# Performance work log

Measured on AMD Instinct MI355X. Metric: run time of the kernel, lower is better.

The kernel has to match this reference:

```python
import jax, jax.numpy as jnp
import numpy as np

N_NODES = 50000
N_EDGES = 800000
FEAT, HID, OUT = 256, 256, 40
N_BATCH = 10000
BN_EPS = 1e-5
DEN_EPS = 1e-16


def setup_inputs() -> dict:
    key = jax.random.key(0)
    ks = jax.random.split(key, 12)
    # small feature scale keeps gaussian kernel exp(-gamma*||dh||^2) well-conditioned
    features = jax.random.normal(ks[0], (N_NODES, FEAT), dtype=jnp.float32) * 0.05
    edge_index = jax.random.randint(ks[1], (2, N_EDGES), 0, N_NODES, dtype=jnp.int64)
    batch_nodes = jax.random.randint(ks[2], (N_BATCH,), 0, N_NODES, dtype=jnp.int64)
    W1 = jax.random.normal(ks[3], (FEAT, HID), dtype=jnp.float32) / np.sqrt(FEAT)
    b1 = jnp.zeros((HID,), dtype=jnp.float32)
    gamma1 = jnp.float32(0.5)
    W2 = jax.random.normal(ks[4], (HID, OUT), dtype=jnp.float32) / np.sqrt(HID)
    b2 = jnp.zeros((OUT,), dtype=jnp.float32)
    gamma2 = jnp.float32(0.5)
    bn1_w = jnp.ones((HID,), dtype=jnp.float32)
    bn1_b = jnp.zeros((HID,), dtype=jnp.float32)
    bn2_w = jnp.ones((OUT,), dtype=jnp.float32)
    bn2_b = jnp.zeros((OUT,), dtype=jnp.float32)
    return dict(features=features, edge_index=edge_index, batch_nodes=batch_nodes,
                W1=W1, b1=b1, gamma1=gamma1, W2=W2, b2=b2, gamma2=gamma2,
                bn1_w=bn1_w, bn1_b=bn1_b, bn2_w=bn2_w, bn2_b=bn2_b)


def pfgcn_conv(x, edge_index, W, b, gamma):
    # linear transform then gaussian-kernel weighted aggregation over edges
    h = x @ W + b                                  # [N, C_out]
    src, dst = edge_index[0], edge_index[1]
    h_src = h[src]                                 # [E, C_out] gather
    h_dst = h[dst]                                 # [E, C_out] gather
    d2 = jnp.sum((h_src - h_dst) ** 2, axis=-1)    # [E]
    w = jnp.exp(-gamma * d2)                       # gaussian edge kernel
    denom = jax.ops.segment_sum(w, dst, num_segments=N_NODES) + DEN_EPS   # [N]
    num = jax.ops.segment_sum(w[:, None] * h_src, dst, num_segments=N_NODES)  # [N, C_out]
    return num / denom[:, None]


def batchnorm(x, g, b):
    # training-mode BatchNorm1d over the node dimension
    mu = jnp.mean(x, axis=0)
    var = jnp.var(x, axis=0)
    return (x - mu) * jax.lax.rsqrt(var + BN_EPS) * g + b


def reference(features, edge_index, batch_nodes, W1, b1, gamma1, W2, b2, gamma2,
              bn1_w, bn1_b, bn2_w, bn2_b):
    x = pfgcn_conv(features, edge_index, W1, b1, gamma1)
    x = jax.nn.relu(batchnorm(x, bn1_w, bn1_b))
    # dropout treated as identity (eval / deterministic reference)
    x = pfgcn_conv(x, edge_index, W2, b2, gamma2)
    x = jax.nn.relu(batchnorm(x, bn2_w, bn2_b))
    return jax.nn.log_softmax(x[batch_nodes], axis=1)
```

## Files before the change

### kernel.cpp

```cpp
#include <hip/hip_runtime.h>
#include <math.h>

#define N_NODES 50000
#define N_EDGES 800000
#define OUTC 40
#define N_BATCH 10000
#define H2S 48
#define BKT 64
#define SP 16

typedef float f32x4 __attribute__((ext_vector_type(4)));
typedef short s16x8 __attribute__((ext_vector_type(8)));
typedef short s16x4 __attribute__((ext_vector_type(4)));

union Frag { s16x8 v; s16x4 h[2]; };

__device__ inline unsigned short f2bf(float f) {
    unsigned int u = __float_as_uint(f);
    u += 0x7fff + ((u >> 16) & 1);
    return (unsigned short)(u >> 16);
}
__device__ inline float lo16(unsigned int u) { return __uint_as_float(u << 16); }
__device__ inline float hi16(unsigned int u) { return __uint_as_float(u & 0xffff0000u); }
__device__ inline unsigned int pk2(float a, float b) {
    return (unsigned int)f2bf(a) | ((unsigned int)f2bf(b) << 16);
}
__device__ inline void unpk8(uint4 u, float* f) {
    f[0] = lo16(u.x); f[1] = hi16(u.x);
    f[2] = lo16(u.y); f[3] = hi16(u.y);
    f[4] = lo16(u.z); f[5] = hi16(u.z);
    f[6] = lo16(u.w); f[7] = hi16(u.w);
}

__global__ __launch_bounds__(256) void init_kernel(const float* __restrict__ W1,
                                                   unsigned short* __restrict__ W1T,
                                                   int* __restrict__ cur,
                                                   float* __restrict__ stats) {
    int b = blockIdx.x, t = threadIdx.x;
    if (b < 256) {
        W1T[(size_t)t * 256 + b] = f2bf(W1[(size_t)b * 256 + t]);
    } else if (b < 256 + 196) {
        int i = (b - 256) * 256 + t;
        if (i < N_NODES) cur[i] = 0;
    } else {
        int base = (b - 452) * 1184;
        for (int i = base + t; i < base + 1184; i += 256)
            if (i < 9472) stats[i] = 0.f;
    }
}

__global__ __launch_bounds__(256) void scatter_kernel(const int* __restrict__ ei,
                                                      int* __restrict__ cur,
                                                      unsigned short* __restrict__ srcs) {
    int e = blockIdx.x * 256 + threadIdx.x;
    if (e >= N_EDGES) return;
    int d = ei[N_EDGES + e];
    int pos = atomicAdd(&cur[d], 1);
    if (pos < BKT) srcs[(size_t)d * BKT + pos] = (unsigned short)ei[e];
}

#define LDA 40
__global__ __launch_bounds__(256) void gemm1_mfma(const float* __restrict__ A,
                                                  const unsigned short* __restrict__ BT,
                                                  const float* __restrict__ bias,
                                                  unsigned short* __restrict__ C) {
    __shared__ unsigned short As[128 * LDA];
    __shared__ unsigned short Bs[128 * LDA];
    int t = threadIdx.x;
    int lane = t & 63, wave = t >> 6;
    int ln = lane & 15, quad = lane >> 4;
    int row0 = blockIdx.x * 128;
    int col0 = blockIdx.y * 128;
    int m0 = (wave & 1) * 64, n0 = (wave >> 1) * 64;
    f32x4 acc[4][4];
    #pragma unroll
    for (int i = 0; i < 4; i++)
        #pragma unroll
        for (int j = 0; j < 4; j++) acc[i][j] = (f32x4){0.f, 0.f, 0.f, 0.f};
    int r = t >> 1, half = t & 1;

    for (int k0 = 0; k0 < 256; k0 += 32) {
        {
            int gr = row0 + r;
            float4 v[4];
            if (gr < N_NODES) {
                const float4* src = (const float4*)(A + (size_t)gr * 256 + k0 + half * 16);
                v[0] = src[0]; v[1] = src[1]; v[2] = src[2]; v[3] = src[3];
            } else {
                float4 z = make_float4(0.f, 0.f, 0.f, 0.f);
                v[0] = z; v[1] = z; v[2] = z; v[3] = z;
            }
            ushort4* dst = (ushort4*)&As[r * LDA + half * 16];
            #pragma unroll
            for (int q = 0; q < 4; q++) {
                ushort4 u;
                u.x = f2bf(v[q].x); u.y = f2bf(v[q].y);
                u.z = f2bf(v[q].z); u.w = f2bf(v[q].w);
                dst[q] = u;
            }
        }
        {
            const ushort4* src = (const ushort4*)(BT + (size_t)(col0 + r) * 256 + k0 + half * 16);
            ushort4* dst = (ushort4*)&Bs[r * LDA + half * 16];
            dst[0] = src[0]; dst[1] = src[1]; dst[2] = src[2]; dst[3] = src[3];
        }
        __syncthreads();
        Frag af[4], bf[4];
        #pragma unroll
        for (int i = 0; i < 4; i++) {
            int ar = m0 + i * 16 + ln;
            af[i].h[0] = *(const s16x4*)&As[ar * LDA + quad * 8];
            af[i].h[1] = *(const s16x4*)&As[ar * LDA + quad * 8 + 4];
            int br = n0 + i * 16 + ln;
            bf[i].h[0] = *(const s16x4*)&Bs[br * LDA + quad * 8];
            bf[i].h[1] = *(const s16x4*)&Bs[br * LDA + quad * 8 + 4];
        }
        #pragma unroll
        for (int i = 0; i < 4; i++)
            #pragma unroll
            for (int j = 0; j < 4; j++)
                acc[i][j] = __builtin_amdgcn_mfma_f32_16x16x32_bf16(af[i].v, bf[j].v, acc[i][j], 0, 0, 0);
        __syncthreads();
    }
    #pragma unroll
    for (int j = 0; j < 4; j++) {
        int gc = col0 + n0 + j * 16 + ln;
        float bv = bias[gc];
        #pragma unroll
        for (int i = 0; i < 4; i++) {
            int gb = row0 + m0 + i * 16 + quad * 4;
            #pragma unroll
            for (int rg = 0; rg < 4; rg++) {
                int gr = gb + rg;
                if (gr < N_NODES) C[(size_t)gr * 256 + gc] = f2bf(acc[i][j][rg] + bv);
            }
        }
    }
}

__global__ __launch_bounds__(256) void agg1_kernel(const unsigned short* __restrict__ h,
                                                   const int* __restrict__ degp,
                                                   const unsigned short* __restrict__ srcs,
                                                   const float* __restrict__ gamma_p,
                                                   unsigned short* __restrict__ x1) {
    int lane = threadIdx.x & 63;
    int node = blockIdx.x * 4 + (threadIdx.x >> 6);
    if (node >= N_NODES) return;
    int eslot = lane >> 4, cgrp = lane & 15;
    float g = gamma_p[0];
    float hd[16];
    {
        const uint4* hrow = (const uint4*)(h + (size_t)node * 256 + cgrp * 16);
        uint4 u0 = hrow[0], u1 = hrow[1];
        unpk8(u0, hd); unpk8(u1, hd + 8);
    }
    float acc[16];
    #pragma unroll
    for (int c = 0; c < 16; c++) acc[c] = 0.f;
    float den = 0.f;
    int beg = node << 6;
    int end = beg + degp[node];
    int n_it = (end - beg + 3) >> 2;
    for (int it = 0; it < n_it; it++) {
        int i = beg + it * 4 + eslot;
        bool valid = i < end;
        int s = valid ? (int)srcs[i] : node;
        const uint4* arow = (const uint4*)(h + (size_t)s * 256 + cgrp * 16);
        uint4 u0 = arow[0], u1 = arow[1];
        float av[16];
        unpk8(u0, av); unpk8(u1, av + 8);
        float d2 = 0.f;
        #pragma unroll
        for (int c = 0; c < 16; c++) { float d = av[c] - hd[c]; d2 = fmaf(d, d, d2); }
        d2 += __shfl_xor(d2, 1, 64);
        d2 += __shfl_xor(d2, 2, 64);
        d2 += __shfl_xor(d2, 4, 64);
        d2 += __shfl_xor(d2, 8, 64);
        float w = valid ? __expf(-g * d2) : 0.f;
        den += w;
        #pragma unroll
        for (int c = 0; c < 16; c++) acc[c] = fmaf(w, av[c], acc[c]);
    }
    #pragma unroll
    for (int m = 16; m < 64; m <<= 1) {
        den += __shfl_xor(den, m, 64);
        #pragma unroll
        for (int c = 0; c < 16; c++) acc[c] += __shfl_xor(acc[c], m, 64);
    }
    if (eslot == 0) {
        float inv = 1.f / (den + 1e-16f);
        float vv[16];
        #pragma unroll
        for (int c = 0; c < 16; c++) vv[c] = acc[c] * inv;
        uint4 oA = make_uint4(pk2(vv[0], vv[1]), pk2(vv[2], vv[3]),
                              pk2(vv[4], vv[5]), pk2(vv[6], vv[7]));
        uint4 oB = make_uint4(pk2(vv[8], vv[9]), pk2(vv[10], vv[11]),
                              pk2(vv[12], vv[13]), pk2(vv[14], vv[15]));
        uint4* o4 = (uint4*)(x1 + (size_t)node * 256 + cgrp * 16);
        o4[0] = oA; o4[1] = oB;
    }
}

__global__ __launch_bounds__(256) void stats1_kernel(const unsigned short* __restrict__ x,
                                                     float* __restrict__ sum,
                                                     float* __restrict__ sumsq) {
    __shared__ float ls[4][256], lq[4][256];
    int t = threadIdx.x;
    int cg = (t & 63) * 4;
    int rs = t >> 6;
    float s0 = 0.f, s1 = 0.f, s2 = 0.f, s3 = 0.f;
    float q0 = 0.f, q1 = 0.f, q2 = 0.f, q3 = 0.f;
    for (int r = blockIdx.x * 4 + rs; r < N_NODES; r += gridDim.x * 4) {
        uint2 u = *(const uint2*)(x + (size_t)r * 256 + cg);
        float v0 = lo16(u.x), v1 = hi16(u.x), v2 = lo16(u.y), v3 = hi16(u.y);
        s0 += v0; q0 = fmaf(v0, v0, q0);
        s1 += v1; q1 = fmaf(v1, v1, q1);
        s2 += v2; q2 = fmaf(v2, v2, q2);
        s3 += v3; q3 = fmaf(v3, v3, q3);
    }
    ls[rs][cg] = s0; ls[rs][cg + 1] = s1; ls[rs][cg + 2] = s2; ls[rs][cg + 3] = s3;
    lq[rs][cg] = q0; lq[rs][cg + 1] = q1; lq[rs][cg + 2] = q2; lq[rs][cg + 3] = q3;
    __syncthreads();
    float S = ls[0][t] + ls[1][t] + ls[2][t] + ls[3][t];
    float Q = lq[0][t] + lq[1][t] + lq[2][t] + lq[3][t];
    atomicAdd(&sum[t * SP], S);
    atomicAdd(&sumsq[t * SP], Q);
}

__global__ __launch_bounds__(256) void gemm2_kernel(const unsigned short* __restrict__ X,
                                                    const float* __restrict__ W2,
                                                    const float* __restrict__ bias,
                                                    const float* __restrict__ sum1,
                                                    const float* __restrict__ sumsq1,
                                                    const float* __restrict__ bg,
                                                    const float* __restrict__ bb,
                                                    unsigned short* __restrict__ H) {
    __shared__ float W2s[40 * 260];
    __shared__ float aas[256], bbs[256];
    int t = threadIdx.x;
    for (int i = t; i < 256 * 40; i += 256) {
        int k = i / 40, c = i % 40;
        W2s[c * 260 + k] = W2[i];
    }
    {
        const float invN = 1.f / N_NODES;
        float mu = sum1[t * SP] * invN;
        float var = sumsq1[t * SP] * invN - mu * mu;
        float rs = rsqrtf(var + 1e-5f) * bg[t];
        aas[t] = rs;
        bbs[t] = bb[t] - mu * rs;
    }
    __syncthreads();
    int slot = t >> 2, cg = t & 3;
    int rbase = blockIdx.x * 256 + slot;
    const uint2* xp[4];
    #pragma unroll
    for (int rr = 0; rr < 4; rr++) xp[rr] = (const uint2*)(X + (size_t)(rbase + rr * 64) * 256);
    float acc[4][10];
    #pragma unroll
    for (int rr = 0; rr < 4; rr++)
        #pragma unroll
        for (int i = 0; i < 10; i++) acc[rr][i] = 0.f;

    for (int k4 = 0; k4 < 64; k4++) {
        int k = k4 * 4;
        float4 a4 = *(const float4*)&aas[k];
        float4 b4 = *(const float4*)&bbs[k];
        float4 w4[10];
        #pragma unroll
        for (int i = 0; i < 10; i++) w4[i] = *(const float4*)&W2s[(cg * 10 + i) * 260 + k];
        #pragma unroll
        for (int rr = 0; rr < 4; rr++) {
            uint2 xu = xp[rr][k4];
            float y0 = fmaxf(fmaf(lo16(xu.x), a4.x, b4.x), 0.f);
            float y1 = fmaxf(fmaf(hi16(xu.x), a4.y, b4.y), 0.f);
            float y2 = fmaxf(fmaf(lo16(xu.y), a4.z, b4.z), 0.f);
            float y3 = fmaxf(fmaf(hi16(xu.y), a4.w, b4.w), 0.f);
            #pragma unroll
            for (int i = 0; i < 10; i++)
                acc[rr][i] += y0 * w4[i].x + y1 * w4[i].y + y2 * w4[i].z + y3 * w4[i].w;
        }
    }
    #pragma unroll
    for (int rr = 0; rr < 4; rr++) {
        int row = rbase + rr * 64;
        if (row < N_NODES) {
            float y[10];
            #pragma unroll
            for (int i = 0; i < 10; i++) y[i] = acc[rr][i] + bias[cg * 10 + i];
            unsigned int* o32 = (unsigned int*)(H + (size_t)row * H2S + cg * 10);
            #pragma unroll
            for (int i = 0; i < 5; i++) o32[i] = pk2(y[2 * i], y[2 * i + 1]);
            if (cg == 1)
                *(uint4*)(H + (size_t)row * H2S + 40) = make_uint4(0, 0, 0, 0);
        }
    }
}

__global__ __launch_bounds__(256) void agg2_kernel(const unsigned short* __restrict__ h,
                                                   const int* __restrict__ degp,
                                                   const unsigned short* __restrict__ srcs,
                                                   const float* __restrict__ gamma_p,
                                                   float* __restrict__ x2) {
    int l32 = threadIdx.x & 31;
    int node = blockIdx.x * 8 + (threadIdx.x >> 5);
    if (node >= N_NODES) return;
    int eslot = l32 >> 3, cgrp = l32 & 7;
    float g = gamma_p[0];
    float hd[6];
    {
        const unsigned int* hrow = (const unsigned int*)(h + (size_t)node * H2S + cgrp * 6);
        unsigned int u0 = hrow[0], u1 = hrow[1], u2 = hrow[2];
        hd[0] = lo16(u0); hd[1] = hi16(u0);
        hd[2] = lo16(u1); hd[3] = hi16(u1);
        hd[4] = lo16(u2); hd[5] = hi16(u2);
    }
    float acc[6] = {0.f, 0.f, 0.f, 0.f, 0.f, 0.f};
    float den = 0.f;
    int beg = node << 6;
    int end = beg + degp[node];
    int n_it = (end - beg + 3) >> 2;
    for (int it = 0; it < n_it; it++) {
        int i = beg + it * 4 + eslot;
        bool valid = i < end;
        int s = valid ? (int)srcs[i] : node;
        const unsigned int* arow = (const unsigned int*)(h + (size_t)s * H2S + cgrp * 6);
        unsigned int u0 = arow[0], u1 = arow[1], u2 = arow[2];
        float av[6];
        av[0] = lo16(u0); av[1] = hi16(u0);
        av[2] = lo16(u1); av[3] = hi16(u1);
        av[4] = lo16(u2); av[5] = hi16(u2);
        float d2 = 0.f;
        #pragma unroll
        for (int j = 0; j < 6; j++) { float d = av[j] - hd[j]; d2 = fmaf(d, d, d2); }
        d2 += __shfl_xor(d2, 1, 64);
        d2 += __shfl_xor(d2, 2, 64);
        d2 += __shfl_xor(d2, 4, 64);
        float w = valid ? __expf(-g * d2) : 0.f;
        den += w;
        #pragma unroll
        for (int j = 0; j < 6; j++) acc[j] = fmaf(w, av[j], acc[j]);
    }
    #pragma unroll
    for (int m = 8; m < 32; m <<= 1) {
        den += __shfl_xor(den, m, 64);
        #pragma unroll
        for (int j = 0; j < 6; j++) acc[j] += __shfl_xor(acc[j], m, 64);
    }
    if (eslot == 0) {
        float inv = 1.f / (den + 1e-16f);
        int cb = cgrp * 6;
        #pragma unroll
        for (int j = 0; j < 6; j++)
            if (cb + j < OUTC) x2[(size_t)node * OUTC + cb + j] = acc[j] * inv;
    }
}

__global__ __launch_bounds__(256) void stats2_kernel(const float* __restrict__ x,
                                                     float* __restrict__ sum,
                                                     float* __restrict__ sumsq) {
    __shared__ float ls[12][40], lq[12][40];
    int t = threadIdx.x;
    if (t < 240) {
        int c2 = (t % 20) * 2;
        int rs = t / 20;
        float s0 = 0.f, s1 = 0.f, q0 = 0.f, q1 = 0.f;
        for (int r = blockIdx.x * 12 + rs; r < N_NODES; r += gridDim.x * 12) {
            float2 v = *(const float2*)(x + (size_t)r * OUTC + c2);
            s0 += v.x; q0 = fmaf(v.x, v.x, q0);
            s1 += v.y; q1 = fmaf(v.y, v.y, q1);
        }
        ls[rs][c2] = s0; ls[rs][c2 + 1] = s1;
        lq[rs][c2] = q0; lq[rs][c2 + 1] = q1;
    }
    __syncthreads();
    if (t < OUTC) {
        float S = 0.f, Q = 0.f;
        #pragma unroll
        for (int rs = 0; rs < 12; rs++) { S += ls[rs][t]; Q += lq[rs][t]; }
        atomicAdd(&sum[t * SP], S);
        atomicAdd(&sumsq[t * SP], Q);
    }
}

__global__ __launch_bounds__(256) void final_kernel(const float* __restrict__ x2,
                                                    const float* __restrict__ sum,
                                                    const float* __restrict__ sumsq,
                                                    const float* __restrict__ g,
                                                    const float* __restrict__ b,
                                                    const int* __restrict__ batch,
                                                    float* __restrict__ out) {
    int lane = threadIdx.x & 63;
    int row = blockIdx.x * 4 + (threadIdx.x >> 6);
    if (row >= N_BATCH) return;
    int node = batch[row];
    bool act = lane < OUTC;
    float v = -INFINITY;
    if (act) {
        const float invN = 1.f / N_NODES;
        float mu = sum[lane * SP] * invN;
        float var = sumsq[lane * SP] * invN - mu * mu;
        float xv = x2[(size_t)node * OUTC + lane];
        float y = (xv - mu) * rsqrtf(var + 1e-5f) * g[lane] + b[lane];
        v = fmaxf(y, 0.f);
    }
    float m = v;
    #pragma unroll
    for (int s = 1; s < 64; s <<= 1) m = fmaxf(m, __shfl_xor(m, s, 64));
    float p = act ? expf(v - m) : 0.f;
    float ssum = p;
    #pragma unroll
    for (int s = 1; s < 64; s <<= 1) ssum += __shfl_xor(ssum, s, 64);
    if (act) out[(size_t)row * OUTC + lane] = v - m - logf(ssum);
}

extern "C" void kernel_launch(void* const* d_in, const int* in_sizes, int n_in,
                              void* d_out, int out_size, void* d_ws, size_t ws_size,
                              hipStream_t stream) {
    const float* feat   = (const float*)d_in[0];
    const int*   ei     = (const int*)d_in[1];
    const int*   batch  = (const int*)d_in[2];
    const float* W1     = (const float*)d_in[3];
    const float* b1     = (const float*)d_in[4];
    const float* gamma1 = (const float*)d_in[5];
    const float* W2     = (const float*)d_in[6];
    const float* b2     = (const float*)d_in[7];
    const float* gamma2 = (const float*)d_in[8];
    const float* bn1w   = (const float*)d_in[9];
    const float* bn1b   = (const float*)d_in[10];
    const float* bn2w   = (const float*)d_in[11];
    const float* bn2b   = (const float*)d_in[12];

    char* ws = (char*)d_ws;
    unsigned short* h1  = (unsigned short*)ws;
    unsigned short* x1  = (unsigned short*)(ws + 25600000);
    unsigned short* srcs = (unsigned short*)(ws + 52000000);
    int* cur            = (int*)(ws + 65600000);
    float* stats        = (float*)(ws + 66000000);
    unsigned short* w1t = (unsigned short*)(ws + 76800000);
    float* sum1   = stats;
    float* sumsq1 = stats + 256 * SP;
    float* sum2   = stats + 512 * SP;
    float* sumsq2 = stats + 512 * SP + 40 * SP;
    unsigned short* h2 = (unsigned short*)ws;
    float* x2 = (float*)(ws + 25600000);
    float* out = (float*)d_out;

    init_kernel<<<460, 256, 0, stream>>>(W1, w1t, cur, stats);
    scatter_kernel<<<(N_EDGES + 255) / 256, 256, 0, stream>>>(ei, cur, srcs);

    gemm1_mfma<<<dim3(391, 2), 256, 0, stream>>>(feat, w1t, b1, h1);
    agg1_kernel<<<(N_NODES + 3) / 4, 256, 0, stream>>>(h1, cur, srcs, gamma1, x1);
    stats1_kernel<<<256, 256, 0, stream>>>(x1, sum1, sumsq1);

    gemm2_kernel<<<196, 256, 0, stream>>>(x1, W2, b2, sum1, sumsq1, bn1w, bn1b, h2);
    agg2_kernel<<<(N_NODES + 7) / 8, 256, 0, stream>>>(h2, cur, srcs, gamma2, x2);
    stats2_kernel<<<256, 256, 0, stream>>>(x2, sum2, sumsq2);
    final_kernel<<<(N_BATCH + 3) / 4, 256, 0, stream>>>(x2, sum2, sumsq2, bn2w, bn2b, batch, out);
}
```

Baseline: 347.6 us.

## Pre-convert features to bf16 in scatter kernel and spread gemm2 over more blocks

The fp32 to bf16 conversion of the node features moves out of gemm1 into extra blocks appended to the edge-scatter launch. The bf16 copy goes into the workspace buffer that x1 uses later. gemm1 then loads bf16 directly, halving its A-tile traffic, though the separate conversion pass adds a full read and write of the features. gemm2 drops from four rows per thread to one and launches 784 blocks instead of 196, for more parallelism at the cost of reloading W2 and the BN parameters into shared memory per block.

Result: slower. 360.3 us (+3.6%).

```diff
diff --git a/kernel.cpp b/kernel.cpp
--- a/kernel.cpp
+++ b/kernel.cpp
@@ -8,6 +8,8 @@
 #define H2S 48
 #define BKT 64
 #define SP 16
+#define SCAT_BLKS 3125
+#define CONV_BLKS 6250
 
 typedef float f32x4 __attribute__((ext_vector_type(4)));
 typedef short s16x8 __attribute__((ext_vector_type(8)));
@@ -49,18 +51,32 @@
     }
 }
 
-__global__ __launch_bounds__(256) void scatter_kernel(const int* __restrict__ ei,
-                                                      int* __restrict__ cur,
-                                                      unsigned short* __restrict__ srcs) {
-    int e = blockIdx.x * 256 + threadIdx.x;
-    if (e >= N_EDGES) return;
-    int d = ei[N_EDGES + e];
-    int pos = atomicAdd(&cur[d], 1);
-    if (pos < BKT) srcs[(size_t)d * BKT + pos] = (unsigned short)ei[e];
+__global__ __launch_bounds__(256) void scatter_conv(const int* __restrict__ ei,
+                                                    int* __restrict__ cur,
+                                                    unsigned short* __restrict__ srcs,
+                                                    const float* __restrict__ feat,
+                                                    unsigned short* __restrict__ fbf) {
+    int b = blockIdx.x, t = threadIdx.x;
+    if (b < SCAT_BLKS) {
+        int e = b * 256 + t;
+        if (e < N_EDGES) {
+            int d = ei[N_EDGES + e];
+            int pos = atomicAdd(&cur[d], 1);
+            if (pos < BKT) srcs[(size_t)d * BKT + pos] = (unsigned short)ei[e];
+        }
+    } else {
+        size_t e8 = ((size_t)(b - SCAT_BLKS) * 256 + t) * 8;
+        const float4* src = (const float4*)(feat + e8);
+        float4 v0 = src[0], v1 = src[1];
+        uint4 o;
+        o.x = pk2(v0.x, v0.y); o.y = pk2(v0.z, v0.w);
+        o.z = pk2(v1.x, v1.y); o.w = pk2(v1.z, v1.w);
+        *(uint4*)(fbf + e8) = o;
+    }
 }
 
 #define LDA 40
-__global__ __launch_bounds__(256) void gemm1_mfma(const float* __restrict__ A,
+__global__ __launch_bounds__(256) void gemm1_mfma(const unsigned short* __restrict__ A,
                                                   const unsigned short* __restrict__ BT,
                                                   const float* __restrict__ bias,
                                                   unsigned short* __restrict__ C) {
@@ -82,21 +98,13 @@
     for (int k0 = 0; k0 < 256; k0 += 32) {
         {
             int gr = row0 + r;
-            float4 v[4];
+            ushort4* dst = (ushort4*)&As[r * LDA + half * 16];
             if (gr < N_NODES) {
-                const float4* src = (const float4*)(A + (size_t)gr * 256 + k0 + half * 16);
-                v[0] = src[0]; v[1] = src[1]; v[2] = src[2]; v[3] = src[3];
+                const ushort4* src = (const ushort4*)(A + (size_t)gr * 256 + k0 + half * 16);
+                dst[0] = src[0]; dst[1] = src[1]; dst[2] = src[2]; dst[3] = src[3];
             } else {
-                float4 z = make_float4(0.f, 0.f, 0.f, 0.f);
-                v[0] = z; v[1] = z; v[2] = z; v[3] = z;
-            }
-            ushort4* dst = (ushort4*)&As[r * LDA + half * 16];
-            #pragma unroll
-            for (int q = 0; q < 4; q++) {
-                ushort4 u;
-                u.x = f2bf(v[q].x); u.y = f2bf(v[q].y);
-                u.z = f2bf(v[q].z); u.w = f2bf(v[q].w);
-                dst[q] = u;
+                ushort4 z = make_ushort4(0, 0, 0, 0);
+                dst[0] = z; dst[1] = z; dst[2] = z; dst[3] = z;
             }
         }
         {
@@ -252,48 +260,36 @@
     }
     __syncthreads();
     int slot = t >> 2, cg = t & 3;
-    int rbase = blockIdx.x * 256 + slot;
-    const uint2* xp[4];
-    #pragma unroll
-    for (int rr = 0; rr < 4; rr++) xp[rr] = (const uint2*)(X + (size_t)(rbase + rr * 64) * 256);
-    float acc[4][10];
-    #pragma unroll
-    for (int rr = 0; rr < 4; rr++)
-        #pragma unroll
-        for (int i = 0; i < 10; i++) acc[rr][i] = 0.f;
+    int row = blockIdx.x * 64 + slot;
+    const uint2* xp = (const uint2*)(X + (size_t)row * 256);
+    float acc[10];
+    #pragma unroll
+    for (int i = 0; i < 10; i++) acc[i] = 0.f;
 
     for (int k4 = 0; k4 < 64; k4++) {
         int k = k4 * 4;
         float4 a4 = *(const float4*)&aas[k];
         float4 b4 = *(const float4*)&bbs[k];
-        float4 w4[10];
-        #pragma unroll
-        for (int i = 0; i < 10; i++) w4[i] = *(const float4*)&W2s[(cg * 10 + i) * 260 + k];
-        #pragma unroll
-        for (int rr = 0; rr < 4; rr++) {
-            uint2 xu = xp[rr][k4];
-            float y0 = fmaxf(fmaf(lo16(xu.x), a4.x, b4.x), 0.f);
-            float y1 = fmaxf(fmaf(hi16(xu.x), a4.y, b4.y), 0.f);
-            float y2 = fmaxf(fmaf(lo16(xu.y), a4.z, b4.z), 0.f);
-            float y3 = fmaxf(fmaf(hi16(xu.y), a4.w, b4.w), 0.f);
-            #pragma unroll
-            for (int i = 0; i < 10; i++)
-                acc[rr][i] += y0 * w4[i].x + y1 * w4[i].y + y2 * w4[i].z + y3 * w4[i].w;
-        }
-    }
-    #pragma unroll
-    for (int rr = 0; rr < 4; rr++) {
-        int row = rbase + rr * 64;
-        if (row < N_NODES) {
-            float y[10];
-            #pragma unroll
-            for (int i = 0; i < 10; i++) y[i] = acc[rr][i] + bias[cg * 10 + i];
-            unsigned int* o32 = (unsigned int*)(H + (size_t)row * H2S + cg * 10);
-            #pragma unroll
-            for (int i = 0; i < 5; i++) o32[i] = pk2(y[2 * i], y[2 * i + 1]);
-            if (cg == 1)
-                *(uint4*)(H + (size_t)row * H2S + 40) = make_uint4(0, 0, 0, 0);
-        }
+        uint2 xu = xp[k4];
+        float y0 = fmaxf(fmaf(lo16(xu.x), a4.x, b4.x), 0.f);
+        float y1 = fmaxf(fmaf(hi16(xu.x), a4.y, b4.y), 0.f);
+        float y2 = fmaxf(fmaf(lo16(xu.y), a4.z, b4.z), 0.f);
+        float y3 = fmaxf(fmaf(hi16(xu.y), a4.w, b4.w), 0.f);
+        #pragma unroll
+        for (int i = 0; i < 10; i++) {
+            float4 w = *(const float4*)&W2s[(cg * 10 + i) * 260 + k];
+            acc[i] += y0 * w.x + y1 * w.y + y2 * w.z + y3 * w.w;
+        }
+    }
+    if (row < N_NODES) {
+        float y[10];
+        #pragma unroll
+        for (int i = 0; i < 10; i++) y[i] = acc[i] + bias[cg * 10 + i];
+        unsigned int* o32 = (unsigned int*)(H + (size_t)row * H2S + cg * 10);
+        #pragma unroll
+        for (int i = 0; i < 5; i++) o32[i] = pk2(y[2 * i], y[2 * i + 1]);
+        if (cg == 1)
+            *(uint4*)(H + (size_t)row * H2S + 40) = make_uint4(0, 0, 0, 0);
     }
 }
 
@@ -434,6 +430,7 @@
     char* ws = (char*)d_ws;
     unsigned short* h1  = (unsigned short*)ws;
     unsigned short* x1  = (unsigned short*)(ws + 25600000);
+    unsigned short* fbf = x1;
     unsigned short* srcs = (unsigned short*)(ws + 52000000);
     int* cur            = (int*)(ws + 65600000);
     float* stats        = (float*)(ws + 66000000);
@@ -447,13 +444,13 @@
     float* out = (float*)d_out;
 
     init_kernel<<<460, 256, 0, stream>>>(W1, w1t, cur, stats);
-    scatter_kernel<<<(N_EDGES + 255) / 256, 256, 0, stream>>>(ei, cur, srcs);
-
-    gemm1_mfma<<<dim3(391, 2), 256, 0, stream>>>(feat, w1t, b1, h1);
+    scatter_conv<<<SCAT_BLKS + CONV_BLKS, 256, 0, stream>>>(ei, cur, srcs, feat, fbf);
+
+    gemm1_mfma<<<dim3(391, 2), 256, 0, stream>>>(fbf, w1t, b1, h1);
     agg1_kernel<<<(N_NODES + 3) / 4, 256, 0, stream>>>(h1, cur, srcs, gamma1, x1);
     stats1_kernel<<<256, 256, 0, stream>>>(x1, sum1, sumsq1);
 
-    gemm2_kernel<<<196, 256, 0, stream>>>(x1, W2, b2, sum1, sumsq1, bn1w, bn1b, h2);
+    gemm2_kernel<<<784, 256, 0, stream>>>(x1, W2, b2, sum1, sumsq1, bn1w, bn1b, h2);
     agg2_kernel<<<(N_NODES + 7) / 8, 256, 0, stream>>>(h2, cur, srcs, gamma2, x2);
     stats2_kernel<<<256, 256, 0, stream>>>(x2, sum2, sumsq2);
     final_kernel<<<(N_BATCH + 3) / 4, 256, 0, stream>>>(x2, sum2, sumsq2, bn2w, bn2b, batch, out);
```
